# Performance work log

Hardware: AMD Instinct MI355X
Metric: run time of the kernel (lower is better)

The kernel has to match this reference:

```python
import jax, jax.numpy as jnp
import numpy as np

B, S, D, H, E, K = 2, 2048, 512, 2048, 16, 2
LN_EPS = 1e-5


def setup_inputs() -> dict:
    key = jax.random.key(0)
    ks = jax.random.split(key, 9)
    s_in = 1.0 / np.sqrt(D)
    s_hid = 1.0 / np.sqrt(H)
    return {
        "x": jax.random.normal(ks[0], (B, S, D), dtype=jnp.float32),
        "Wg": jax.random.normal(ks[1], (D, E), dtype=jnp.float32) * s_in,
        "bg": jax.random.normal(ks[2], (E,), dtype=jnp.float32) * 0.01,
        "W1": jax.random.normal(ks[3], (E, D, H), dtype=jnp.float32) * s_in,
        "b1": jax.random.normal(ks[4], (E, H), dtype=jnp.float32) * 0.01,
        "W2": jax.random.normal(ks[5], (E, H, D), dtype=jnp.float32) * s_hid,
        "b2": jax.random.normal(ks[6], (E, D), dtype=jnp.float32) * 0.01,
        "gamma": jnp.ones((D,), dtype=jnp.float32),
        "beta": jnp.zeros((D,), dtype=jnp.float32),
    }


def reference(x, Wg, bg, W1, b1, W2, b2, gamma, beta):
    # --- top-k gating (GatingFuncTopK) ---
    logits = jnp.einsum("bsd,de->bse", x, Wg) + bg            # [B,S,E]
    probs = jax.nn.softmax(logits, axis=-1)
    topk_vals, topk_idx = jax.lax.top_k(probs, K)             # [B,S,K]
    # scatter top-k probs back into a sparse [B,S,E] routing matrix
    sparse = (jax.nn.one_hot(topk_idx, E, dtype=probs.dtype)
              * topk_vals[..., None]).sum(axis=-2)            # [B,S,E]

    # --- dense all-expert FFN (stack over experts, as in the torch code) ---
    h = jax.nn.relu(jnp.einsum("bsd,edh->ebsh", x, W1)
                    + b1[:, None, None, :])                   # [E,B,S,H]
    ex = jnp.einsum("ebsh,ehd->ebsd", h, W2) + b2[:, None, None, :]  # [E,B,S,D]

    # --- weighted combine + residual + layernorm ---
    out = jnp.einsum("bse,ebsd->bsd", sparse, ex) + x
    mu = out.mean(axis=-1, keepdims=True)
    var = ((out - mu) ** 2).mean(axis=-1, keepdims=True)
    out = (out - mu) * jax.lax.rsqrt(var + LN_EPS) * gamma + beta
    return out
```

## Files before the change

kernel.cpp:

```cpp
#include <hip/hip_runtime.h>
#include <math.h>

#define NTOK 4096
#define DDIM 512
#define HDIM 2048
#define NEXP 16


#define WS_COUNTS    0u
#define WS_EPOS      4096u
#define WS_TOK       36864u
#define WS_WL        299008u
#define WS_XA        1048576u
#define WS_W1T       11534336u
#define WS_W2T       45088768u
#define WS_HB        78643200u
#define WS_YB        WS_W1T

typedef __attribute__((ext_vector_type(8))) short short8;
typedef __attribute__((ext_vector_type(4))) float floatx4;
typedef unsigned short ushort_t;

__device__ __forceinline__ ushort_t f2bf(float f) {
    unsigned u = __float_as_uint(f);
    u += 0x7fffu + ((u >> 16) & 1u);
    return (ushort_t)(u >> 16);
}
__device__ __forceinline__ float bf2f(ushort_t u) {
    return __uint_as_float((unsigned)u << 16);
}
__device__ __forceinline__ unsigned pk2(float a, float b) {
    return (unsigned)f2bf(a) | ((unsigned)f2bf(b) << 16);
}

__device__ __forceinline__ void gld16(const void* g, void* l) {
    __builtin_amdgcn_global_load_lds(
        (const __attribute__((address_space(1))) unsigned*)g,
        (__attribute__((address_space(3))) unsigned*)l, 16, 0, 0);
}

#define WAIT4_BAR() asm volatile("s_waitcnt vmcnt(4)\n\ts_barrier" ::: "memory")
#define WAIT0_BAR() asm volatile("s_waitcnt vmcnt(0)\n\ts_barrier" ::: "memory")

struct TileInfo { int e, m0, Me, aoff, total; };
__device__ __forceinline__ TileInfo tile_lookup(const int* __restrict__ counts,
                                                int t)
{
    TileInfo ti; ti.e = 0; ti.m0 = 0; ti.Me = 0; ti.aoff = 0;
    int total = 0, aacc = 0;
    #pragma unroll
    for (int j = 0; j < NEXP; ++j) {
        const int c = counts[j * 16];
        const int tj = (c + 127) >> 7;
        if (t >= total && t < total + tj) {
            ti.e = j; ti.m0 = (t - total) << 7; ti.Me = c; ti.aoff = aacc;
        }
        total += tj;
        aacc += c;
    }
    ti.total = total;
    return ti;
}

__device__ __forceinline__ void wtrans_tile(
    const float* __restrict__ src, ushort_t* __restrict__ dst,
    int C, int NT, int CK, int e, int ks, int nw, unsigned* lb, int tid)
{
    const int q = tid >> 4;
    const int c0 = (tid & 15) << 2;
    const float* sp = src + (size_t)e * (DDIM * HDIM)
                    + (size_t)(ks * 32 + 2 * q) * C + nw * 256;
    float4 va[4], vb[4];
    #pragma unroll
    for (int p = 0; p < 4; ++p) {
        va[p] = *(const float4*)(sp + c0 + p * 64);
        vb[p] = *(const float4*)(sp + C + c0 + p * 64);
    }
    #pragma unroll
    for (int p = 0; p < 4; ++p) {
        const int n = c0 + p * 64;
        lb[(n + 0) * 17 + q] = pk2(va[p].x, vb[p].x);
        lb[(n + 1) * 17 + q] = pk2(va[p].y, vb[p].y);
        lb[(n + 2) * 17 + q] = pk2(va[p].z, vb[p].z);
        lb[(n + 3) * 17 + q] = pk2(va[p].w, vb[p].w);
    }
    __syncthreads();
    const int nt = tid >> 4, nl = tid & 15;
    const int ntg = nw * 16 + nt;
    ushort_t* rbase = dst + ((size_t)e * NT + ntg) * ((size_t)CK * 128) + nl * 8;
    const unsigned* rp = lb + (nt * 16 + nl) * 17;
    #pragma unroll
    for (int kc = 0; kc < 4; ++kc) {
        const unsigned o0 = rp[kc * 4 + 0], o1 = rp[kc * 4 + 1];
        const unsigned o2 = rp[kc * 4 + 2], o3 = rp[kc * 4 + 3];
        *(uint4*)(rbase + (size_t)(ks * 4 + kc) * 128) = make_uint4(o0, o1, o2, o3);
    }
}

__global__ __launch_bounds__(256) void fusedA_kernel(
    const float* __restrict__ x, const float* __restrict__ Wg,
    const float* __restrict__ bg, int* __restrict__ counts,
    int* __restrict__ tok_list, float* __restrict__ w_list,
    int* __restrict__ epos, const float* __restrict__ W1,
    ushort_t* __restrict__ W1t)
{
    __shared__ __align__(16) float smem[4416];
    __shared__ int lcnt[16], lbase[16];
    const int tid = threadIdx.x;
    int bid = blockIdx.x;

    if (bid >= 512) {
        bid -= 512;
        const int e = bid >> 7, r = bid & 127;
        const int nw = r & 7, ks = r >> 3;
        wtrans_tile(W1, W1t, HDIM, 128, 64, e, ks, nw, (unsigned*)smem, tid);
        return;
    }

    float (*xs)[520] = (float(*)[520])smem;
    float (*lsm)[16][2] = (float(*)[16][2])(smem + 4160);
    const int t0 = bid * 8;
    const float* xg = x + (size_t)t0 * DDIM;
    #pragma unroll
    for (int p = 0; p < 4; ++p) {
        const int idx = p * 1024 + tid * 4;
        *(float4*)&xs[idx >> 9][idx & 511] = *(const float4*)(xg + idx);
    }
    if (tid < 16) lcnt[tid] = 0;
    __syncthreads();
    const int tl = tid >> 5, e = (tid >> 1) & 15, h = tid & 1;
    float a0 = 0.f, a1 = 0.f, a2 = 0.f, a3 = 0.f;
    #pragma unroll 8
    for (int it = 0; it < 64; ++it) {
        const int d = h * 256 + it * 4;
        const float4 xv = *(const float4*)&xs[tl][d];
        a0 = fmaf(xv.x, Wg[(d + 0) * 16 + e], a0);
        a1 = fmaf(xv.y, Wg[(d + 1) * 16 + e], a1);
        a2 = fmaf(xv.z, Wg[(d + 2) * 16 + e], a2);
        a3 = fmaf(xv.w, Wg[(d + 3) * 16 + e], a3);
    }
    lsm[tl][e][h] = (a0 + a1) + (a2 + a3);
    __syncthreads();

    int i0 = 0, i1 = -1, r0 = 0, r1 = 0;
    float w0 = 0.f, w1 = 0.f;
    const bool tokth = ((tid & 31) == 0);
    if (tokth) {
        float l[16];
        #pragma unroll
        for (int j = 0; j < NEXP; ++j) l[j] = lsm[tl][j][0] + lsm[tl][j][1] + bg[j];
        float m = -1e30f;
        #pragma unroll
        for (int j = 0; j < NEXP; ++j) m = fmaxf(m, l[j]);
        float s = 0.f;
        #pragma unroll
        for (int j = 0; j < NEXP; ++j) s += __expf(l[j] - m);
        float v0 = -1e30f;
        #pragma unroll
        for (int j = 0; j < NEXP; ++j)
            if (l[j] > v0) { v0 = l[j]; i0 = j; }
        float v1 = -1e30f;
        #pragma unroll
        for (int j = 0; j < NEXP; ++j)
            if (j != i0 && l[j] > v1) { v1 = l[j]; i1 = j; }
        w0 = __expf(v0 - m) / s;
        w1 = __expf(v1 - m) / s;
        r0 = atomicAdd(&lcnt[i0], 1);
        r1 = atomicAdd(&lcnt[i1], 1);
    }
    __syncthreads();
    if (tid < 16 && lcnt[tid] > 0)
        lbase[tid] = atomicAdd(&counts[tid * 16], lcnt[tid]);
    __syncthreads();
    if (tokth) {
        const int t = t0 + tl;
        const int p0 = lbase[i0] + r0;
        tok_list[i0 * NTOK + p0] = t;
        w_list[i0 * NTOK + p0] = w0;
        epos[t * 2 + 0] = (i0 << 16) | p0;
        const int p1 = lbase[i1] + r1;
        tok_list[i1 * NTOK + p1] = t;
        w_list[i1 * NTOK + p1] = w1;
        epos[t * 2 + 1] = (i1 << 16) | p1;
    }
}

__global__ __launch_bounds__(256) void gather_xa(
    const float* __restrict__ x, const int* __restrict__ tok_list,
    const int* __restrict__ counts, ushort_t* __restrict__ xa)
{
    const int b = blockIdx.x;
    const TileInfo ti = tile_lookup(counts, b);
    if (b >= ti.total) return;
    const int e = ti.e, m0 = ti.m0, Me = ti.Me;
    const int row = threadIdx.x >> 1;
    const int half = threadIdx.x & 1;
    const int kbase = blockIdx.y * 128 + half * 64;
    const int tok = tok_list[e * NTOK + min(m0 + row, Me - 1)];
    const float* src = x + (size_t)tok * DDIM + kbase;
    ushort_t* dstb = xa + (size_t)b * 65536 + (size_t)(row >> 4) * 8192 + (row & 15) * 8;
    #pragma unroll
    for (int q = 0; q < 16; ++q) {
        const int k = kbase + q * 4;
        const float4 v = *(const float4*)(src + q * 4);
        ushort4 o = make_ushort4(f2bf(v.x), f2bf(v.y), f2bf(v.z), f2bf(v.w));
        *(ushort4*)(dstb + (size_t)(k >> 3) * 128 + (k & 7)) = o;
    }
}

__global__ __launch_bounds__(256) void fusedC_kernel(
    const ushort_t* __restrict__ xa, const ushort_t* __restrict__ W1t,
    const float* __restrict__ b1, const int* __restrict__ counts,
    ushort_t* __restrict__ hb,
    const float* __restrict__ W2, ushort_t* __restrict__ W2t)
{
    __shared__ __align__(16) ushort_t lds[24576];
    const int tid = threadIdx.x;
    const int bid = blockIdx.x;

    if (bid >= 1280) {
        const int wb = bid - 1280;
        const int e = wb >> 7, r = wb & 127;
        const int nw = r & 1, ks = r >> 1;
        wtrans_tile(W2, W2t, DDIM, 32, 256, e, ks, nw, (unsigned*)lds, tid);
        return;
    }

    const int swz = (bid & 7) * 160 + (bid >> 3);
    const int t = swz >> 4;
    const TileInfo ti = tile_lookup(counts, t);
    if (t >= ti.total) return;
    const int e = ti.e;
    const int n0 = (swz & 15) << 7;
    const int lane = tid & 63, w = tid >> 6;
    const int fm = lane & 15, fq = lane >> 4;
    const int wr = (w >> 1) << 6, wc = (w & 1) << 6;

    const ushort_t* gA = xa + (size_t)t * 65536 + lane * 8;
    const ushort_t* gB = W1t + ((size_t)e * 128 + (n0 >> 4)) * 8192 + lane * 8;
    const int s0 = w, s1 = w + 4;

    #define G1_STAGE(d, kc) do {                                            \
        ushort_t* lb_ = &lds[(d) * 8192];                                   \
        gld16(gA + (size_t)s0 * 8192 + (kc) * 512, lb_ + s0 * 512);         \
        gld16(gA + (size_t)s1 * 8192 + (kc) * 512, lb_ + s1 * 512);         \
        gld16(gB + (size_t)s0 * 8192 + (kc) * 512, lb_ + 4096 + s0 * 512);  \
        gld16(gB + (size_t)s1 * 8192 + (kc) * 512, lb_ + 4096 + s1 * 512);  \
    } while (0)

    #define G1_COMPUTE(cur) do {                                            \
        const ushort_t* la = &lds[(cur) * 8192 + ((w >> 1) * 4) * 512 + lane * 8]; \
        const ushort_t* lbB = &lds[(cur) * 8192 + 4096 + ((w & 1) * 4) * 512 + lane * 8]; \
        short8 af[4], bf[4];                                                \
        _Pragma("unroll")                                                   \
        for (int i = 0; i < 4; ++i) af[i] = *(const short8*)(la + i * 512); \
        _Pragma("unroll")                                                   \
        for (int j = 0; j < 4; ++j) bf[j] = *(const short8*)(lbB + j * 512);\
        _Pragma("unroll")                                                   \
        for (int i = 0; i < 4; ++i)                                         \
            _Pragma("unroll")                                               \
            for (int j = 0; j < 4; ++j)                                     \
                acc[i][j] = __builtin_amdgcn_mfma_f32_16x16x32_bf16(        \
                    af[i], bf[j], acc[i][j], 0, 0, 0);                      \
    } while (0)

    G1_STAGE(0, 0);
    G1_STAGE(1, 1);
    floatx4 acc[4][4] = {};
    int cur = 0;
    #pragma unroll 1
    for (int kc = 0; kc < 14; ++kc) {
        WAIT4_BAR();
        const int nb = (kc + 2) % 3;
        G1_STAGE(nb, kc + 2);
        G1_COMPUTE(cur);
        cur = (cur == 2) ? 0 : cur + 1;
    }
    WAIT4_BAR();
    G1_COMPUTE(cur);
    cur = (cur == 2) ? 0 : cur + 1;
    WAIT0_BAR();
    G1_COMPUTE(cur);
    __syncthreads();
    #undef G1_STAGE
    #undef G1_COMPUTE

    ushort_t* ls = lds;
    #pragma unroll
    for (int j = 0; j < 4; ++j) {
        const float bias = b1[(size_t)e * HDIM + n0 + wc + j * 16 + fm];
        #pragma unroll
        for (int i = 0; i < 4; ++i)
            #pragma unroll
            for (int r = 0; r < 4; ++r) {
                const int row = wr + i * 16 + fq * 4 + r;
                ls[row * 128 + wc + j * 16 + fm] =
                    f2bf(fmaxf(acc[i][j][r] + bias, 0.f));
            }
    }
    __syncthreads();
    ushort_t* hbase = hb + (size_t)t * 262144 + (size_t)(n0 >> 3) * 128;
    #pragma unroll
    for (int p = 0; p < 8; ++p) {
        const int unit = tid + p * 256;
        const int row = unit >> 4, c16 = unit & 15;
        *(short8*)(hbase + (size_t)(row >> 4) * 32768 + (size_t)c16 * 128
                   + (row & 15) * 8) = *(const short8*)&ls[row * 128 + c16 * 8];
    }
}

__global__ __launch_bounds__(256) void gemm2_mfma(
    const ushort_t* __restrict__ hb, const ushort_t* __restrict__ W2t,
    const float* __restrict__ b2, const float* __restrict__ w_list,
    const int* __restrict__ counts, ushort_t* __restrict__ yb)
{
    const int bid = blockIdx.x;
    const int swz = (bid & 7) * 160 + (bid >> 3);
    const int n0i = swz & 3;
    const int q_ = swz >> 2;
    const int kz = q_ / 80;
    const int t = q_ - kz * 80;
    const TileInfo ti = tile_lookup(counts, t);
    if (t >= ti.total) return;
    const int e = ti.e, m0 = ti.m0, Me = ti.Me, aoff = ti.aoff;
    const int n0 = n0i << 7;
    const int tid = threadIdx.x, lane = tid & 63, w = tid >> 6;
    const int fm = lane & 15, fq = lane >> 4;
    const int wr = (w >> 1) << 6, wc = (w & 1) << 6;

    __shared__ __align__(16) ushort_t lds[24576];

    const ushort_t* gA = hb + (size_t)t * 262144 + (size_t)kz * 8192 + lane * 8;
    const ushort_t* gB = W2t + ((size_t)e * 32 + (n0 >> 4)) * 32768
                       + (size_t)kz * 8192 + lane * 8;
    const int s0 = w, s1 = w + 4;

    #define G2_STAGE(d, kc) do {                                            \
        ushort_t* lb_ = &lds[(d) * 8192];                                   \
        gld16(gA + (size_t)s0 * 32768 + (kc) * 512, lb_ + s0 * 512);        \
        gld16(gA + (size_t)s1 * 32768 + (kc) * 512, lb_ + s1 * 512);        \
        gld16(gB + (size_t)s0 * 32768 + (kc) * 512, lb_ + 4096 + s0 * 512); \
        gld16(gB + (size_t)s1 * 32768 + (kc) * 512, lb_ + 4096 + s1 * 512); \
    } while (0)

    #define G2_COMPUTE(cur) do {                                            \
        const ushort_t* la = &lds[(cur) * 8192 + ((w >> 1) * 4) * 512 + lane * 8]; \
        const ushort_t* lbB = &lds[(cur) * 8192 + 4096 + ((w & 1) * 4) * 512 + lane * 8]; \
        short8 af[4], bf[4];                                                \
        _Pragma("unroll")                                                   \
        for (int i = 0; i < 4; ++i) af[i] = *(const short8*)(la + i * 512); \
        _Pragma("unroll")                                                   \
        for (int j = 0; j < 4; ++j) bf[j] = *(const short8*)(lbB + j * 512);\
        _Pragma("unroll")                                                   \
        for (int i = 0; i < 4; ++i)                                         \
            _Pragma("unroll")                                               \
            for (int j = 0; j < 4; ++j)                                     \
                acc[i][j] = __builtin_amdgcn_mfma_f32_16x16x32_bf16(        \
                    af[i], bf[j], acc[i][j], 0, 0, 0);                      \
    } while (0)

    G2_STAGE(0, 0);
    G2_STAGE(1, 1);
    floatx4 acc[4][4] = {};
    int cur = 0;
    #pragma unroll 1
    for (int kc = 0; kc < 14; ++kc) {
        WAIT4_BAR();
        const int nb = (kc + 2) % 3;
        G2_STAGE(nb, kc + 2);
        G2_COMPUTE(cur);
        cur = (cur == 2) ? 0 : cur + 1;
    }
    WAIT4_BAR();
    G2_COMPUTE(cur);
    cur = (cur == 2) ? 0 : cur + 1;
    WAIT0_BAR();
    G2_COMPUTE(cur);
    __syncthreads();
    #undef G2_STAGE
    #undef G2_COMPUTE

    ushort_t* ls = lds;
    #pragma unroll
    for (int j = 0; j < 4; ++j) {
        const float bias = (kz == 0) ? b2[(size_t)e * DDIM + n0 + wc + j * 16 + fm] : 0.f;
        #pragma unroll
        for (int i = 0; i < 4; ++i)
            #pragma unroll
            for (int r = 0; r < 4; ++r) {
                const int row = wr + i * 16 + fq * 4 + r;
                const float gw = w_list[e * NTOK + min(m0 + row, Me - 1)];
                ls[row * 128 + wc + j * 16 + fm] = f2bf(gw * (acc[i][j][r] + bias));
            }
    }
    __syncthreads();
    ushort_t* ybase = yb + (size_t)kz * (8192 * 512) + n0;
    #pragma unroll
    for (int p = 0; p < 8; ++p) {
        const int unit = tid + p * 256;
        const int row = unit >> 4, c16 = unit & 15;
        if (m0 + row < Me)
            *(short8*)(ybase + (size_t)(aoff + m0 + row) * 512 + c16 * 8)
                = *(const short8*)&ls[row * 128 + c16 * 8];
    }
}

__global__ __launch_bounds__(256) void ln_kernel(
    const float* __restrict__ x, const ushort_t* __restrict__ yb,
    const int* __restrict__ epos, const int* __restrict__ counts,
    const float* __restrict__ gamma, const float* __restrict__ beta,
    float* __restrict__ out)
{
    const int t = blockIdx.x * 4 + (threadIdx.x >> 6);
    const int lane = threadIdx.x & 63;
    const int d0 = lane * 8;

    const int p0 = epos[2 * t + 0];
    const int p1 = epos[2 * t + 1];
    const int e0 = p0 >> 16, e1 = p1 >> 16;
    int off0 = 0, off1 = 0;
    #pragma unroll
    for (int j = 0; j < NEXP; ++j) {
        const int c = counts[j * 16];
        off0 += (j < e0) ? c : 0;
        off1 += (j < e1) ? c : 0;
    }
    const size_t r0 = (size_t)(off0 + (p0 & 0xFFFF));
    const size_t r1 = (size_t)(off1 + (p1 & 0xFFFF));

    short8 ys[8];
    #pragma unroll
    for (int kz = 0; kz < 4; ++kz) {
        ys[kz * 2 + 0] = *(const short8*)(yb + (size_t)kz * (8192 * 512) + r0 * 512 + d0);
        ys[kz * 2 + 1] = *(const short8*)(yb + (size_t)kz * (8192 * 512) + r1 * 512 + d0);
    }
    float xv[8];
    *(float4*)&xv[0] = *(const float4*)(x + (size_t)t * DDIM + d0);
    *(float4*)&xv[4] = *(const float4*)(x + (size_t)t * DDIM + d0 + 4);

    float v[8];
    float s = 0.f;
    #pragma unroll
    for (int i = 0; i < 8; ++i) {
        float a = xv[i];
        #pragma unroll
        for (int q = 0; q < 8; ++q) a += bf2f((ushort_t)ys[q][i]);
        v[i] = a;
        s += a;
    }
    #pragma unroll
    for (int o = 32; o > 0; o >>= 1) s += __shfl_xor(s, o, 64);
    const float mu = s * (1.f / DDIM);
    float q = 0.f;
    #pragma unroll
    for (int i = 0; i < 8; ++i) { const float d_ = v[i] - mu; q = fmaf(d_, d_, q); }
    #pragma unroll
    for (int o = 32; o > 0; o >>= 1) q += __shfl_xor(q, o, 64);
    const float rstd = rsqrtf(q * (1.f / DDIM) + 1e-5f);

    float g[8], bt[8], o8[8];
    *(float4*)&g[0] = *(const float4*)(gamma + d0);
    *(float4*)&g[4] = *(const float4*)(gamma + d0 + 4);
    *(float4*)&bt[0] = *(const float4*)(beta + d0);
    *(float4*)&bt[4] = *(const float4*)(beta + d0 + 4);
    #pragma unroll
    for (int i = 0; i < 8; ++i) o8[i] = (v[i] - mu) * rstd * g[i] + bt[i];
    *(float4*)(out + (size_t)t * DDIM + d0) = *(float4*)&o8[0];
    *(float4*)(out + (size_t)t * DDIM + d0 + 4) = *(float4*)&o8[4];
}

extern "C" void kernel_launch(void* const* d_in, const int* in_sizes, int n_in,
                              void* d_out, int out_size, void* d_ws, size_t ws_size,
                              hipStream_t stream) {
    const float* x     = (const float*)d_in[0];
    const float* Wg    = (const float*)d_in[1];
    const float* bg    = (const float*)d_in[2];
    const float* W1    = (const float*)d_in[3];
    const float* b1    = (const float*)d_in[4];
    const float* W2    = (const float*)d_in[5];
    const float* b2    = (const float*)d_in[6];
    const float* gamma = (const float*)d_in[7];
    const float* beta  = (const float*)d_in[8];
    float* out = (float*)d_out;

    char* ws = (char*)d_ws;
    int*      counts   = (int*)(ws + WS_COUNTS);
    int*      epos     = (int*)(ws + WS_EPOS);
    int*      tok_list = (int*)(ws + WS_TOK);
    float*    w_list   = (float*)(ws + WS_WL);
    ushort_t* xa       = (ushort_t*)(ws + WS_XA);
    ushort_t* W1t      = (ushort_t*)(ws + WS_W1T);
    ushort_t* W2t      = (ushort_t*)(ws + WS_W2T);
    ushort_t* hb       = (ushort_t*)(ws + WS_HB);
    ushort_t* yb       = (ushort_t*)(ws + WS_YB);

    hipMemsetAsync(counts, 0, 1024, stream);
    fusedA_kernel<<<2560, 256, 0, stream>>>(x, Wg, bg, counts, tok_list, w_list,
                                            epos, W1, W1t);
    gather_xa<<<dim3(80, 4), 256, 0, stream>>>(x, tok_list, counts, xa);
    fusedC_kernel<<<3328, 256, 0, stream>>>(xa, W1t, b1, counts, hb, W2, W2t);
    gemm2_mfma<<<1280, 256, 0, stream>>>(hb, W2t, b2, w_list, counts, yb);
    ln_kernel<<<NTOK / 4, 256, 0, stream>>>(x, yb, epos, counts, gamma, beta, out);
}
```

Baseline: 264.5 us.

## Fold token gather into GEMM1 A-loads and convert x to bf16 in routing kernel

The separate gather_xa launch, which copied routed token rows into a tiled bf16 buffer, is removed. The routing kernel now also writes a dense bf16 copy of x, and the first expert GEMM loads A rows directly through tok_list indirection. This drops one kernel launch and one intermediate write/read pass, at the cost of less contiguous A loads in the GEMM. MFMA sections are also wrapped with s_setprio to favour matrix issue.

```diff
diff --git a/kernel.cpp b/kernel.cpp
--- a/kernel.cpp
+++ b/kernel.cpp
@@ -11,7 +11,7 @@
 #define WS_EPOS      4096u
 #define WS_TOK       36864u
 #define WS_WL        299008u
-#define WS_XA        1048576u
+#define WS_XBF       1048576u
 #define WS_W1T       11534336u
 #define WS_W2T       45088768u
 #define WS_HB        78643200u
@@ -102,7 +102,7 @@
     const float* __restrict__ bg, int* __restrict__ counts,
     int* __restrict__ tok_list, float* __restrict__ w_list,
     int* __restrict__ epos, const float* __restrict__ W1,
-    ushort_t* __restrict__ W1t)
+    ushort_t* __restrict__ W1t, ushort_t* __restrict__ xbf)
 {
     __shared__ __align__(16) float smem[4416];
     __shared__ int lcnt[16], lbase[16];
@@ -128,6 +128,18 @@
     }
     if (tid < 16) lcnt[tid] = 0;
     __syncthreads();
+
+    {
+        const int row = tid >> 5, col = (tid & 31) * 16;
+        const float* sr = &xs[row][col];
+        unsigned o[8];
+        #pragma unroll
+        for (int j = 0; j < 8; ++j) o[j] = pk2(sr[2 * j], sr[2 * j + 1]);
+        ushort_t* xd = xbf + (size_t)(t0 + row) * DDIM + col;
+        *(uint4*)(xd) = make_uint4(o[0], o[1], o[2], o[3]);
+        *(uint4*)(xd + 8) = make_uint4(o[4], o[5], o[6], o[7]);
+    }
+
     const int tl = tid >> 5, e = (tid >> 1) & 15, h = tid & 1;
     float a0 = 0.f, a1 = 0.f, a2 = 0.f, a3 = 0.f;
     #pragma unroll 8
@@ -185,33 +197,10 @@
     }
 }
 
-__global__ __launch_bounds__(256) void gather_xa(
-    const float* __restrict__ x, const int* __restrict__ tok_list,
-    const int* __restrict__ counts, ushort_t* __restrict__ xa)
-{
-    const int b = blockIdx.x;
-    const TileInfo ti = tile_lookup(counts, b);
-    if (b >= ti.total) return;
-    const int e = ti.e, m0 = ti.m0, Me = ti.Me;
-    const int row = threadIdx.x >> 1;
-    const int half = threadIdx.x & 1;
-    const int kbase = blockIdx.y * 128 + half * 64;
-    const int tok = tok_list[e * NTOK + min(m0 + row, Me - 1)];
-    const float* src = x + (size_t)tok * DDIM + kbase;
-    ushort_t* dstb = xa + (size_t)b * 65536 + (size_t)(row >> 4) * 8192 + (row & 15) * 8;
-    #pragma unroll
-    for (int q = 0; q < 16; ++q) {
-        const int k = kbase + q * 4;
-        const float4 v = *(const float4*)(src + q * 4);
-        ushort4 o = make_ushort4(f2bf(v.x), f2bf(v.y), f2bf(v.z), f2bf(v.w));
-        *(ushort4*)(dstb + (size_t)(k >> 3) * 128 + (k & 7)) = o;
-    }
-}
-
 __global__ __launch_bounds__(256) void fusedC_kernel(
-    const ushort_t* __restrict__ xa, const ushort_t* __restrict__ W1t,
-    const float* __restrict__ b1, const int* __restrict__ counts,
-    ushort_t* __restrict__ hb,
+    const ushort_t* __restrict__ xbf, const int* __restrict__ tok_list,
+    const ushort_t* __restrict__ W1t, const float* __restrict__ b1,
+    const int* __restrict__ counts, ushort_t* __restrict__ hb,
     const float* __restrict__ W2, ushort_t* __restrict__ W2t)
 {
     __shared__ __align__(16) ushort_t lds[24576];
@@ -230,20 +219,26 @@
     const int t = swz >> 4;
     const TileInfo ti = tile_lookup(counts, t);
     if (t >= ti.total) return;
-    const int e = ti.e;
+    const int e = ti.e, m0 = ti.m0, Me = ti.Me;
     const int n0 = (swz & 15) << 7;
     const int lane = tid & 63, w = tid >> 6;
     const int fm = lane & 15, fq = lane >> 4;
     const int wr = (w >> 1) << 6, wc = (w & 1) << 6;
 
-    const ushort_t* gA = xa + (size_t)t * 65536 + lane * 8;
+    const int rtA = 2 * w, rtB = 2 * w + 1;
+    const int arow = lane & 15, akq = lane >> 4;
+    const int tokA = tok_list[e * NTOK + min(m0 + rtA * 16 + arow, Me - 1)];
+    const int tokB = tok_list[e * NTOK + min(m0 + rtB * 16 + arow, Me - 1)];
+    const ushort_t* gA0 = xbf + (size_t)tokA * DDIM + akq * 8;
+    const ushort_t* gA1 = xbf + (size_t)tokB * DDIM + akq * 8;
+
     const ushort_t* gB = W1t + ((size_t)e * 128 + (n0 >> 4)) * 8192 + lane * 8;
     const int s0 = w, s1 = w + 4;
 
     #define G1_STAGE(d, kc) do {                                            \
         ushort_t* lb_ = &lds[(d) * 8192];                                   \
-        gld16(gA + (size_t)s0 * 8192 + (kc) * 512, lb_ + s0 * 512);         \
-        gld16(gA + (size_t)s1 * 8192 + (kc) * 512, lb_ + s1 * 512);         \
+        gld16(gA0 + (kc) * 32, lb_ + rtA * 512);                            \
+        gld16(gA1 + (kc) * 32, lb_ + rtB * 512);                            \
         gld16(gB + (size_t)s0 * 8192 + (kc) * 512, lb_ + 4096 + s0 * 512);  \
         gld16(gB + (size_t)s1 * 8192 + (kc) * 512, lb_ + 4096 + s1 * 512);  \
     } while (0)
@@ -256,12 +251,14 @@
         for (int i = 0; i < 4; ++i) af[i] = *(const short8*)(la + i * 512); \
         _Pragma("unroll")                                                   \
         for (int j = 0; j < 4; ++j) bf[j] = *(const short8*)(lbB + j * 512);\
+        __builtin_amdgcn_s_setprio(1);                                      \
         _Pragma("unroll")                                                   \
         for (int i = 0; i < 4; ++i)                                         \
             _Pragma("unroll")                                               \
             for (int j = 0; j < 4; ++j)                                     \
                 acc[i][j] = __builtin_amdgcn_mfma_f32_16x16x32_bf16(        \
                     af[i], bf[j], acc[i][j], 0, 0, 0);                      \
+        __builtin_amdgcn_s_setprio(0);                                      \
     } while (0)
 
     G1_STAGE(0, 0);
@@ -488,7 +485,7 @@
     int*      epos     = (int*)(ws + WS_EPOS);
     int*      tok_list = (int*)(ws + WS_TOK);
     float*    w_list   = (float*)(ws + WS_WL);
-    ushort_t* xa       = (ushort_t*)(ws + WS_XA);
+    ushort_t* xbf      = (ushort_t*)(ws + WS_XBF);
     ushort_t* W1t      = (ushort_t*)(ws + WS_W1T);
     ushort_t* W2t      = (ushort_t*)(ws + WS_W2T);
     ushort_t* hb       = (ushort_t*)(ws + WS_HB);
@@ -496,9 +493,9 @@
 
     hipMemsetAsync(counts, 0, 1024, stream);
     fusedA_kernel<<<2560, 256, 0, stream>>>(x, Wg, bg, counts, tok_list, w_list,
-                                            epos, W1, W1t);
-    gather_xa<<<dim3(80, 4), 256, 0, stream>>>(x, tok_list, counts, xa);
-    fusedC_kernel<<<3328, 256, 0, stream>>>(xa, W1t, b1, counts, hb, W2, W2t);
+                                            epos, W1, W1t, xbf);
+    fusedC_kernel<<<3328, 256, 0, stream>>>(xbf, tok_list, W1t, b1, counts, hb,
+                                            W2, W2t);
     gemm2_mfma<<<1280, 256, 0, stream>>>(hb, W2t, b2, w_list, counts, yb);
     ln_kernel<<<NTOK / 4, 256, 0, stream>>>(x, yb, epos, counts, gamma, beta, out);
 }
```

New measurement: 265.3 us. No clear change (+0.3%).
